# Kernel tuning notes

Hardware: AMD Instinct MI355X
Metric: run time of the kernel (lower is better)

## Reference

```python
import jax, jax.numpy as jnp
from jax import lax
import numpy as np

NUM_CLASS = 80
N_PROP = 256
C_FEAT, H_FEAT, W_FEAT = 1024, 50, 80
IMG_H, IMG_W = 800, 1280
POOL = 14
SPATIAL_SCALE = 0.0625
SCORE_THR = 0.5
NMS_THR = 0.7
K_PRE = 1000   # pre-NMS candidate cap (jit-static stand-in for boolean filter)
K_OUT = 200    # keep[:200] in source
BW = (10.0, 10.0, 5.0, 5.0)
SCALE_CLAMP = float(np.log(1000.0 / 16.0))


def setup_inputs() -> dict:
    key = jax.random.key(0)
    ks = jax.random.split(key, 9)
    features = jax.random.normal(ks[0], (1, C_FEAT, H_FEAT, W_FEAT), jnp.float32)
    x1 = jax.random.uniform(ks[1], (N_PROP,), minval=0.0, maxval=IMG_W - 64.0)
    y1 = jax.random.uniform(ks[2], (N_PROP,), minval=0.0, maxval=IMG_H - 64.0)
    w = jax.random.uniform(ks[3], (N_PROP,), minval=32.0, maxval=320.0)
    h = jax.random.uniform(ks[4], (N_PROP,), minval=32.0, maxval=320.0)
    proposals = jnp.stack([x1, y1, jnp.minimum(x1 + w, float(IMG_W)),
                           jnp.minimum(y1 + h, float(IMG_H))], axis=1)
    d_in = C_FEAT * POOL * POOL
    w_fc = jax.random.normal(ks[5], (d_in, 1024), jnp.float32) / np.sqrt(d_in)
    b_fc = jnp.zeros((1024,), jnp.float32)
    # scale class head up so softmax produces confident (>0.5) detections
    w_cls = jax.random.normal(ks[6], (1024, NUM_CLASS + 1), jnp.float32) * (8.0 / np.sqrt(1024))
    b_cls = jnp.zeros((NUM_CLASS + 1,), jnp.float32)
    w_box = jax.random.normal(ks[7], (1024, NUM_CLASS * 4), jnp.float32) / np.sqrt(1024)
    b_box = jnp.zeros((NUM_CLASS * 4,), jnp.float32)
    return {"features": features, "proposals": proposals, "w_fc": w_fc, "b_fc": b_fc,
            "w_cls": w_cls, "b_cls": b_cls, "w_box": w_box, "b_box": b_box}


def roi_align(features, rois):
    """torchvision RoIAlign (aligned=False), output 14x14, one sample per bin.
    features: [1,C,H,W], rois: [N,4] xyxy. Returns [N,C,14,14]."""
    f = features[0]                               # [C,H,W]
    H, W = f.shape[1], f.shape[2]
    x1 = rois[:, 0] * SPATIAL_SCALE
    y1 = rois[:, 1] * SPATIAL_SCALE
    x2 = rois[:, 2] * SPATIAL_SCALE
    y2 = rois[:, 3] * SPATIAL_SCALE
    rw = jnp.maximum(x2 - x1, 1.0)
    rh = jnp.maximum(y2 - y1, 1.0)
    bw = rw / POOL
    bh = rh / POOL
    grid = jnp.arange(POOL, dtype=jnp.float32) + 0.5
    xs = x1[:, None] + grid[None, :] * bw[:, None]      # [N,P] bin-center x
    ys = y1[:, None] + grid[None, :] * bh[:, None]      # [N,P] bin-center y
    Y = jnp.broadcast_to(ys[:, :, None], (rois.shape[0], POOL, POOL))
    X = jnp.broadcast_to(xs[:, None, :], (rois.shape[0], POOL, POOL))
    valid = (Y >= -1.0) & (Y <= H) & (X >= -1.0) & (X <= W)
    y = jnp.clip(Y, 0.0, H - 1.0)
    x = jnp.clip(X, 0.0, W - 1.0)
    y0 = jnp.floor(y).astype(jnp.int32)
    x0 = jnp.floor(x).astype(jnp.int32)
    y1i = jnp.minimum(y0 + 1, H - 1)
    x1i = jnp.minimum(x0 + 1, W - 1)
    ly = y - y0; lx = x - x0; hy = 1.0 - ly; hx = 1.0 - lx
    g = lambda yi, xi: f[:, yi, xi]               # -> [C,N,P,P]
    val = ((hy * hx) * g(y0, x0) + (hy * lx) * g(y0, x1i)
           + (ly * hx) * g(y1i, x0) + (ly * lx) * g(y1i, x1i))
    val = val * valid.astype(val.dtype)
    return jnp.transpose(val, (1, 0, 2, 3))       # [N,C,P,P]


def apply_deltas(boxes, deltas):
    """boxes,deltas: [..., 4]; detectron-style delta apply with weights BW."""
    w = boxes[..., 2] - boxes[..., 0]
    h = boxes[..., 3] - boxes[..., 1]
    cx = boxes[..., 0] + 0.5 * w
    cy = boxes[..., 1] + 0.5 * h
    dx = deltas[..., 0] / BW[0]
    dy = deltas[..., 1] / BW[1]
    dw = jnp.minimum(deltas[..., 2] / BW[2], SCALE_CLAMP)
    dh = jnp.minimum(deltas[..., 3] / BW[3], SCALE_CLAMP)
    pcx = dx * w + cx
    pcy = dy * h + cy
    pw = jnp.exp(dw) * w
    ph = jnp.exp(dh) * h
    return jnp.stack([pcx - 0.5 * pw, pcy - 0.5 * ph,
                      pcx + 0.5 * pw, pcy + 0.5 * ph], axis=-1)


def _iou_matrix(b):
    area = jnp.maximum(b[:, 2] - b[:, 0], 0.0) * jnp.maximum(b[:, 3] - b[:, 1], 0.0)
    lt = jnp.maximum(b[:, None, :2], b[None, :, :2])
    rb = jnp.minimum(b[:, None, 2:], b[None, :, 2:])
    wh = jnp.clip(rb - lt, 0.0)
    inter = wh[..., 0] * wh[..., 1]
    return inter / jnp.maximum(area[:, None] + area[None, :] - inter, 1e-9)


def forward(features, proposals, w_fc, b_fc, w_cls, b_cls, w_box, b_box):
    feat = roi_align(features, proposals)                 # [N,1024,14,14]
    x = feat.reshape(feat.shape[0], -1) @ w_fc + b_fc     # [N,1024]
    logits = x @ w_cls + b_cls                            # [N,81]
    deltas = x @ w_box + b_box                            # [N,320]
    scores = jax.nn.softmax(logits, axis=-1)[:, 1:]       # [N,80] drop bg

    # per-class box-delta apply (proposal expanded over classes)
    boxes = apply_deltas(jnp.broadcast_to(proposals[:, None, :], (N_PROP, NUM_CLASS, 4)),
                         deltas.reshape(N_PROP, NUM_CLASS, 4))
    boxes = jnp.stack([jnp.clip(boxes[..., 0], 0.0, float(IMG_W)),
                       jnp.clip(boxes[..., 1], 0.0, float(IMG_H)),
                       jnp.clip(boxes[..., 2], 0.0, float(IMG_W)),
                       jnp.clip(boxes[..., 3], 0.0, float(IMG_H))], axis=-1)

    # flatten (proposal, class) candidates; mask = score > 0.5 (boolean filter in source)
    s_flat = scores.reshape(-1)
    b_flat = boxes.reshape(-1, 4)
    c_flat = jnp.broadcast_to(jnp.arange(NUM_CLASS)[None, :], (N_PROP, NUM_CLASS)).reshape(-1)
    masked = jnp.where(s_flat > SCORE_THR, s_flat, -1.0)
    top_s, top_i = lax.top_k(masked, K_PRE)              # score-sorted candidates
    cand_b = b_flat[top_i]
    cand_c = c_flat[top_i]
    cand_valid = top_s > SCORE_THR

    # batched NMS: offset boxes by class so classes never interact
    off = cand_c.astype(jnp.float32) * float(IMG_W + 1)
    iou = _iou_matrix(cand_b + off[:, None])
    idxs = jnp.arange(K_PRE)

    def body(keep, xs):
        i, row = xs
        kept_i = keep[i]
        suppress = kept_i & (row > NMS_THR) & (idxs > i)
        return keep & ~suppress, kept_i

    _, kept = lax.scan(body, cand_valid, (idxs, iou))

    # compact kept candidates (already score-ordered) into top-200 slots
    rank = jnp.cumsum(kept.astype(jnp.int32)) - 1
    slot = jnp.where(kept, rank, K_OUT)  # out-of-range -> dropped
    out_boxes = jnp.zeros((K_OUT, 4), cand_b.dtype).at[slot].set(cand_b, mode='drop')
    out_scores = jnp.zeros((K_OUT,), top_s.dtype).at[slot].set(top_s, mode='drop')
    out_classes = jnp.full((K_OUT,), -1, jnp.int32).at[slot].set(cand_c.astype(jnp.int32), mode='drop')
    return out_boxes, out_scores, out_classes


def reference(features, proposals, w_fc, b_fc, w_cls, b_cls, w_box, b_box):
    return forward(features, proposals, w_fc, b_fc, w_cls, b_cls, w_box, b_box)
```

## Files before the change

### kernel.cpp

```cpp
#include <hip/hip_runtime.h>
#include <math.h>

#define N_PROP 256
#define NUM_CLASS 80
#define H_FEAT 50
#define W_FEAT 80
#define K_DIM 200704
#define D_HID 1024
#define SPATIAL_SCALE 0.0625f
#define SCALE_CLAMP 4.135166556742356f
#define IMG_W_F 1280.0f
#define IMG_H_F 800.0f

typedef unsigned short ushort_t;
typedef __attribute__((ext_vector_type(8))) short short8v;
typedef __attribute__((ext_vector_type(16))) float f32x16;
typedef __attribute__((ext_vector_type(4))) float f32x4v;
typedef __attribute__((ext_vector_type(4))) unsigned short ushort4v;
typedef __attribute__((ext_vector_type(2))) unsigned short ushort2v;

__device__ __forceinline__ unsigned short f2bf(float f) {
  unsigned int u = __builtin_bit_cast(unsigned int, f);
  u += 0x7FFFu + ((u >> 16) & 1u);
  return (unsigned short)(u >> 16);
}
__device__ __forceinline__ float bf2f(unsigned short h) {
  unsigned int u = ((unsigned int)h) << 16;
  return __builtin_bit_cast(float, u);
}

__global__ void roi_kernel(const float* __restrict__ F, const float* __restrict__ props,
                           ushort_t* __restrict__ Ahi, ushort_t* __restrict__ Alo) {
  const int tid = threadIdx.x;
  const int m = blockIdx.y;
  const int cg = blockIdx.x;
  __shared__ float w00[196], w01[196], w10[196], w11[196];
  __shared__ int o00[196], o01[196], o10[196], o11[196];
  const float x1s = props[m*4+0]*SPATIAL_SCALE;
  const float y1s = props[m*4+1]*SPATIAL_SCALE;
  const float x2s = props[m*4+2]*SPATIAL_SCALE;
  const float y2s = props[m*4+3]*SPATIAL_SCALE;
  const float bwf = fmaxf(x2s-x1s, 1.0f) / 14.0f;
  const float bhf = fmaxf(y2s-y1s, 1.0f) / 14.0f;
  if (tid < 196) {
    int ph = tid / 14, pw = tid - ph*14;
    float X = x1s + (pw + 0.5f)*bwf;
    float Y = y1s + (ph + 0.5f)*bhf;
    bool valid = (Y >= -1.0f) && (Y <= (float)H_FEAT) && (X >= -1.0f) && (X <= (float)W_FEAT);
    float x = fminf(fmaxf(X, 0.0f), (float)(W_FEAT-1));
    float y = fminf(fmaxf(Y, 0.0f), (float)(H_FEAT-1));
    float xf = floorf(x), yf = floorf(y);
    int ix0 = (int)xf, iy0 = (int)yf;
    int ix1 = min(ix0+1, W_FEAT-1), iy1 = min(iy0+1, H_FEAT-1);
    float lx = x-xf, ly = y-yf, hx = 1.0f-lx, hy = 1.0f-ly;
    float v = valid ? 1.0f : 0.0f;
    w00[tid] = hy*hx*v; w01[tid] = hy*lx*v; w10[tid] = ly*hx*v; w11[tid] = ly*lx*v;
    o00[tid] = iy0*W_FEAT+ix0; o01[tid] = iy0*W_FEAT+ix1;
    o10[tid] = iy1*W_FEAT+ix0; o11[tid] = iy1*W_FEAT+ix1;
  }
  __syncthreads();
  const int base_c = cg*128;
  const size_t rowbase = (size_t)m*K_DIM + (size_t)base_c*196;
  for (int it = 0; it < 49; ++it) {
    int i2 = it*512 + tid*2;
    int c = i2 / 196;
    int b = i2 - c*196;
    const float* f = F + (size_t)(base_c + c)*4000;
    float v0 = w00[b]*f[o00[b]] + w01[b]*f[o01[b]] + w10[b]*f[o10[b]] + w11[b]*f[o11[b]];
    float v1 = w00[b+1]*f[o00[b+1]] + w01[b+1]*f[o01[b+1]] + w10[b+1]*f[o10[b+1]] + w11[b+1]*f[o11[b+1]];
    unsigned short h0 = f2bf(v0), h1 = f2bf(v1);
    ushort2v hv; hv[0] = h0; hv[1] = h1;
    ushort2v lv; lv[0] = f2bf(v0 - bf2f(h0)); lv[1] = f2bf(v1 - bf2f(h1));
    *(ushort2v*)&Ahi[rowbase + i2] = hv;
    *(ushort2v*)&Alo[rowbase + i2] = lv;
  }
}

__global__ __launch_bounds__(512, 2) void mfma_gemm(
    const ushort_t* __restrict__ Ahi, const ushort_t* __restrict__ Alo,
    const float* __restrict__ B, float* __restrict__ P, int steps_per, int nwg) {
  __shared__ ushort_t lds[32768];
  const int tid = threadIdx.x;
  const int wv = tid >> 6, lane = tid & 63, l31 = lane & 31, lhi = lane >> 5;
  const int wm = wv >> 2, wn = wv & 3;
  int id = blockIdx.x;
  int nid = ((nwg & 7) == 0) ? ((id & 7) * (nwg >> 3) + (id >> 3)) : id;
  const int bn = (nid & 3) * 256;
  const int z  = nid >> 2;
  const int step0 = z * steps_per;
  int steps = steps_per;
  if (step0 + steps > 6272) steps = 6272 - step0;

  f32x16 acc[4][2];
  #pragma unroll
  for (int a = 0; a < 4; ++a)
    #pragma unroll
    for (int b = 0; b < 2; ++b)
      #pragma unroll
      for (int e = 0; e < 16; ++e) acc[a][b][e] = 0.0f;

  if (steps > 0) {
    const int H = steps * 2;
    const ushort_t* asrc[2];
    #pragma unroll
    for (int i = 0; i < 2; ++i) {
      int s = i*512 + tid;
      int plane = s >> 9, kb = (s >> 8) & 1, row = s & 255;
      const ushort_t* basep = plane ? Alo : Ahi;
      asrc[i] = basep + (size_t)row * K_DIM + step0*32 + kb*8;
    }
    const int p = tid >> 6, c4 = tid & 63;
    const bool bstage = (tid < 256);
    const float* bsrc = B + (size_t)(step0*32 + 4*p) * D_HID + bn + c4*4;
    const unsigned bkbh = (unsigned)(p >> 1) * 2048u, bsub = (unsigned)((p & 1) * 4);

    #define STAGE_A(bufn) do { \
      _Pragma("unroll") \
      for (int i = 0; i < 2; ++i) { \
        __builtin_amdgcn_global_load_lds(asrc[i], &lds[(bufn) + (unsigned)(i*512 + tid)*8u], 16, 0, 0); \
        asrc[i] += 16; } \
    } while (0)

    #define LOAD_B() do { \
      if (bstage) { \
        b0 = __builtin_nontemporal_load((const f32x4v*)(bsrc)); \
        b1 = __builtin_nontemporal_load((const f32x4v*)(bsrc + D_HID)); \
        b2 = __builtin_nontemporal_load((const f32x4v*)(bsrc + 2*D_HID)); \
        b3 = __builtin_nontemporal_load((const f32x4v*)(bsrc + 3*D_HID)); \
      } \
      bsrc += 16 * D_HID; \
    } while (0)

    #define WRITE_B(bufn) do { \
      if (bstage) { \
        _Pragma("unroll") \
        for (int cc = 0; cc < 4; ++cc) { \
          float g0 = b0[cc], g1 = b1[cc], g2 = b2[cc], g3 = b3[cc]; \
          ushort4v hv, lv; \
          hv[0]=f2bf(g0); lv[0]=f2bf(g0-bf2f(hv[0])); \
          hv[1]=f2bf(g1); lv[1]=f2bf(g1-bf2f(hv[1])); \
          hv[2]=f2bf(g2); lv[2]=f2bf(g2-bf2f(hv[2])); \
          hv[3]=f2bf(g3); lv[3]=f2bf(g3-bf2f(hv[3])); \
          int col = c4*4 + cc, scol = col ^ ((col>>3)&7); \
          unsigned idx = (bufn) + 8192u + bkbh + (unsigned)scol*8u + bsub; \
          *(ushort4v*)&lds[idx] = hv; \
          *(ushort4v*)&lds[idx + 4096] = lv; \
        } \
      } \
    } while (0)

    #define COMPUTE(bufn) do { \
      short8v ah[4], al[4], bh[2], bl[2]; \
      _Pragma("unroll") \
      for (int ms = 0; ms < 4; ++ms) { \
        unsigned ai = (bufn) + (unsigned)(lhi*2048 + (wm*128 + ms*32 + l31)*8); \
        ah[ms] = *(const short8v*)&lds[ai]; \
        al[ms] = *(const short8v*)&lds[ai + 4096]; \
      } \
      _Pragma("unroll") \
      for (int ns = 0; ns < 2; ++ns) { \
        int col = wn*64 + ns*32 + l31, scol = col ^ ((col>>3)&7); \
        unsigned bi = (bufn) + 8192u + (unsigned)(lhi*2048 + scol*8); \
        bh[ns] = *(const short8v*)&lds[bi]; \
        bl[ns] = *(const short8v*)&lds[bi + 4096]; \
      } \
      __builtin_amdgcn_s_setprio(1); \
      _Pragma("unroll") \
      for (int ms = 0; ms < 4; ++ms) \
        _Pragma("unroll") \
        for (int ns = 0; ns < 2; ++ns) { \
          acc[ms][ns] = __builtin_amdgcn_mfma_f32_32x32x16_bf16(ah[ms], bh[ns], acc[ms][ns], 0, 0, 0); \
          acc[ms][ns] = __builtin_amdgcn_mfma_f32_32x32x16_bf16(ah[ms], bl[ns], acc[ms][ns], 0, 0, 0); \
          acc[ms][ns] = __builtin_amdgcn_mfma_f32_32x32x16_bf16(al[ms], bh[ns], acc[ms][ns], 0, 0, 0); \
        } \
      __builtin_amdgcn_s_setprio(0); \
    } while (0)

    f32x4v b0, b1, b2, b3;
    STAGE_A(0u);
    LOAD_B();
    WRITE_B(0u);
    __syncthreads();
    unsigned cur = 0;
    for (int h = 0; h < H; ++h) {
      const bool last = (h == H - 1);
      if (!last) {
        STAGE_A(cur ^ 16384u);
        LOAD_B();
      }
      COMPUTE(cur);
      if (!last) WRITE_B(cur ^ 16384u);
      __syncthreads();
      cur ^= 16384u;
    }
    #undef STAGE_A
    #undef LOAD_B
    #undef WRITE_B
    #undef COMPUTE
  }
  float* Pp = P + (size_t)z * (N_PROP * D_HID);
  #pragma unroll
  for (int ms = 0; ms < 4; ++ms)
    #pragma unroll
    for (int ns = 0; ns < 2; ++ns)
      #pragma unroll
      for (int r = 0; r < 16; ++r) {
        int row = wm*128 + ms*32 + (r & 3) + 8*(r >> 2) + 4*lhi;
        int col = bn + wn*64 + ns*32 + l31;
        __builtin_nontemporal_store(acc[ms][ns][r], &Pp[(size_t)row * D_HID + col]);
      }
}

__global__ void reduce_kernel(const float* __restrict__ P, float* __restrict__ X, int ksplit) {
  int i = blockIdx.x*256 + threadIdx.x;
  f32x4v s = {0.0f, 0.0f, 0.0f, 0.0f};
  const f32x4v* P4 = (const f32x4v*)P;
  for (int r = 0; r < ksplit; ++r) s += P4[(size_t)r*65536 + i];
  ((f32x4v*)X)[i] = s;
}

__global__ void heads_kernel(const float* __restrict__ X, const float* __restrict__ bfc,
                             const float* __restrict__ wcls, const float* __restrict__ bcls,
                             const float* __restrict__ wbox, const float* __restrict__ bbox,
                             float* __restrict__ scores, float* __restrict__ deltas,
                             float* __restrict__ keym) {
  const int tid = threadIdx.x, m = blockIdx.x;
  __shared__ float xs[1024];
  __shared__ float lg[81];
  __shared__ float red[2];
  #pragma unroll
  for (int r = 0; r < 4; ++r) {
    int k = r*256 + tid;
    xs[k] = X[m*1024 + k] + bfc[k];
  }
  __syncthreads();
  for (int j = tid; j < 401; j += 256) {
    if (j < 81) {
      const float* w = wcls + j;
      float accv = bcls[j];
      #pragma unroll 8
      for (int k = 0; k < 1024; ++k) accv = fmaf(xs[k], w[(size_t)k*81], accv);
      lg[j] = accv;
    } else {
      int jb = j - 81;
      const float* w = wbox + jb;
      float accv = bbox[jb];
      #pragma unroll 8
      for (int k = 0; k < 1024; ++k) accv = fmaf(xs[k], w[(size_t)k*320], accv);
      deltas[m*320 + jb] = accv;
    }
  }
  __syncthreads();
  if (tid == 0) {
    float mx = lg[0]; int amax = 0;
    for (int j = 1; j < 81; ++j) if (lg[j] > mx) { mx = lg[j]; amax = j; }
    float sm = 0.0f;
    for (int j = 0; j < 81; ++j) sm += expf(lg[j]-mx);
    float m2 = -1e30f;
    for (int j = 0; j < 81; ++j) if (j != amax) m2 = fmaxf(m2, lg[j]);
    float s2 = 0.0f;
    for (int j = 0; j < 81; ++j) if (j != amax) s2 += expf(lg[j]-m2);
    keym[m] = (m2 - mx) + logf(s2);
    red[0] = mx; red[1] = sm;
  }
  __syncthreads();
  if (tid < 80) scores[m*80 + tid] = expf(lg[tid+1]-red[0]) / red[1];
}

__global__ void detect_kernel(const float* __restrict__ scores, const float* __restrict__ deltas,
                              const float* __restrict__ props, const float* __restrict__ keym,
                              float* __restrict__ out) {
  const int tid = threadIdx.x;
  __shared__ int s_cnt;
  __shared__ float g_key[256];
  __shared__ float g_score[256];
  __shared__ int   g_idx[256];
  __shared__ float c_score[256];
  __shared__ int   c_idx[256];
  __shared__ float bxs[256][4];
  __shared__ int   bcls[256];
  __shared__ unsigned long long supp[256][4];
  __shared__ unsigned char keptf[256];
  __shared__ short slotv[256];
  if (tid == 0) s_cnt = 0;
  g_key[tid] = 1e30f; g_score[tid] = -1.0f; g_idx[tid] = 0x7FFFFFFF;
  c_score[tid] = -1.0f; c_idx[tid] = 0x7FFFFFFF;
  bxs[tid][0] = bxs[tid][1] = bxs[tid][2] = bxs[tid][3] = 0.0f;
  bcls[tid] = 0; keptf[tid] = 0; slotv[tid] = 0;
  __syncthreads();
  for (int t = 0; t < 80; ++t) {
    int i = t*256 + tid;
    float s = scores[i];
    if (s > 0.5f) {
      int p = atomicAdd(&s_cnt, 1);
      if (p < 256) { g_score[p] = s; g_idx[p] = i; g_key[p] = keym[i/80]; }
    }
  }
  __syncthreads();
  const int C = min(s_cnt, 256);
  if (tid < C) {
    float kt = g_key[tid]; int si = g_idx[tid]; float st = g_score[tid];
    int rank = 0;
    for (int u = 0; u < C; ++u) {
      float ku = g_key[u]; int iu = g_idx[u];
      if ((ku < kt) || (ku == kt && iu < si)) ++rank;
    }
    c_score[rank] = st; c_idx[rank] = si;
  }
  __syncthreads();
  if (tid < C) {
    int fi = c_idx[tid];
    int m = fi / 80, j = fi - m*80;
    float px1 = props[m*4+0], py1 = props[m*4+1], px2 = props[m*4+2], py2 = props[m*4+3];
    float w = px2-px1, h = py2-py1;
    float cx = px1 + 0.5f*w, cy = py1 + 0.5f*h;
    const float* d = deltas + m*320 + j*4;
    float dx = d[0]/10.0f, dy = d[1]/10.0f;
    float dw = fminf(d[2]/5.0f, SCALE_CLAMP), dh = fminf(d[3]/5.0f, SCALE_CLAMP);
    float pcx = dx*w + cx, pcy = dy*h + cy;
    float pw = expf(dw)*w, ph = expf(dh)*h;
    bxs[tid][0] = fminf(fmaxf(pcx - 0.5f*pw, 0.0f), IMG_W_F);
    bxs[tid][1] = fminf(fmaxf(pcy - 0.5f*ph, 0.0f), IMG_H_F);
    bxs[tid][2] = fminf(fmaxf(pcx + 0.5f*pw, 0.0f), IMG_W_F);
    bxs[tid][3] = fminf(fmaxf(pcy + 0.5f*ph, 0.0f), IMG_H_F);
    bcls[tid] = j;
  }
  __syncthreads();
  unsigned long long row[4] = {0,0,0,0};
  if (tid < C) {
    float ax1=bxs[tid][0], ay1=bxs[tid][1], ax2=bxs[tid][2], ay2=bxs[tid][3];
    float aarea = fmaxf(ax2-ax1,0.f)*fmaxf(ay2-ay1,0.f);
    int acl = bcls[tid];
    for (int j2 = tid+1; j2 < C; ++j2) {
      if (bcls[j2] != acl) continue;
      float b1=bxs[j2][0], b2=bxs[j2][1], b3=bxs[j2][2], b4=bxs[j2][3];
      float barea = fmaxf(b3-b1,0.f)*fmaxf(b4-b2,0.f);
      float iw = fmaxf(fminf(ax2,b3) - fmaxf(ax1,b1), 0.f);
      float ih = fmaxf(fminf(ay2,b4) - fmaxf(ay1,b2), 0.f);
      float inter = iw*ih;
      float iou = inter / fmaxf(aarea + barea - inter, 1e-9f);
      if (iou > 0.7f) row[j2>>6] |= (1ull << (j2 & 63));
    }
  }
  supp[tid][0]=row[0]; supp[tid][1]=row[1]; supp[tid][2]=row[2]; supp[tid][3]=row[3];
  __syncthreads();
  if (tid == 0) {
    unsigned long long rem[4] = {0,0,0,0};
    int oc = 0;
    for (int i = 0; i < C; ++i) {
      if ((rem[i>>6] >> (i & 63)) & 1ull) continue;
      keptf[i] = 1; slotv[i] = (short)oc;
      ++oc;
      rem[0]|=supp[i][0]; rem[1]|=supp[i][1]; rem[2]|=supp[i][2]; rem[3]|=supp[i][3];
    }
  }
  __syncthreads();
  for (int i = tid; i < 1200; i += 256) out[i] = (i >= 1000) ? -1.0f : 0.0f;
  __syncthreads();
  if (tid < C && keptf[tid] && slotv[tid] < 200) {
    int oc = slotv[tid];
    out[oc*4+0]=bxs[tid][0]; out[oc*4+1]=bxs[tid][1];
    out[oc*4+2]=bxs[tid][2]; out[oc*4+3]=bxs[tid][3];
    out[800+oc]  = c_score[tid];
    out[1000+oc] = (float)bcls[tid];
  }
}

extern "C" void kernel_launch(void* const* d_in, const int* in_sizes, int n_in,
                              void* d_out, int out_size, void* d_ws, size_t ws_size,
                              hipStream_t stream) {
  const float* F     = (const float*)d_in[0];
  const float* props = (const float*)d_in[1];
  const float* wfc   = (const float*)d_in[2];
  const float* bfc   = (const float*)d_in[3];
  const float* wcls  = (const float*)d_in[4];
  const float* bcls  = (const float*)d_in[5];
  const float* wbox  = (const float*)d_in[6];
  const float* bbox  = (const float*)d_in[7];
  float* out = (float*)d_out;
  char* wsb  = (char*)d_ws;

  const size_t abytes = (size_t)N_PROP * K_DIM * 2;
  ushort_t* Ahi = (ushort_t*)wsb;
  ushort_t* Alo = (ushort_t*)(wsb + abytes);
  float* X  = (float*)(wsb + 2*abytes);
  float* SC = X + 262144;
  float* DL = SC + 20480;
  float* KM = DL + 81920;
  float* P  = KM + 256;
  const size_t fixed = 2*abytes + (size_t)(262144 + 20480 + 81920 + 256) * 4;
  if (ws_size < fixed + 2u*1048576u) {
    (void)hipMemsetAsync(d_out, 0x7F, (size_t)out_size*sizeof(float), stream);
    return;
  }
  int ksplit = (int)((ws_size - fixed) / ((size_t)N_PROP * D_HID * 4));
  if (ksplit > 128) ksplit = 128;
  if (ksplit >= 8) ksplit &= ~7;
  const int steps_per = (6272 + ksplit - 1) / ksplit;
  const int nwg = 4 * ksplit;

  roi_kernel   <<<dim3(8, N_PROP),    256, 0, stream>>>(F, props, Ahi, Alo);
  mfma_gemm    <<<nwg,                512, 0, stream>>>(Ahi, Alo, wfc, P, steps_per, nwg);
  reduce_kernel<<<256,                256, 0, stream>>>(P, X, ksplit);
  heads_kernel <<<N_PROP,             256, 0, stream>>>(X, bfc, wcls, bcls, wbox, bbox, SC, DL, KM);
  detect_kernel<<<1,                  256, 0, stream>>>(SC, DL, props, KM, out);
}
```

Before: 851.6 us.

## Fuse split-K reduction into heads kernel, widen RoI stores, cap ksplit at 64

Drops the separate reduce kernel. The heads kernel now sums the split-K partials straight from P, which removes one launch and the X buffer round trip. The RoI kernel now covers 256 channels per block and writes 4-element bf16 vectors in place of pairs, halving the grid. The split-K cap falls from 128 to 64, which gives fewer partials to reduce but less GEMM parallelism.

```diff
diff --git a/kernel.cpp b/kernel.cpp
--- a/kernel.cpp
+++ b/kernel.cpp
@@ -17,7 +17,6 @@
 typedef __attribute__((ext_vector_type(16))) float f32x16;
 typedef __attribute__((ext_vector_type(4))) float f32x4v;
 typedef __attribute__((ext_vector_type(4))) unsigned short ushort4v;
-typedef __attribute__((ext_vector_type(2))) unsigned short ushort2v;
 
 __device__ __forceinline__ unsigned short f2bf(float f) {
   unsigned int u = __builtin_bit_cast(unsigned int, f);
@@ -59,20 +58,23 @@
     o10[tid] = iy1*W_FEAT+ix0; o11[tid] = iy1*W_FEAT+ix1;
   }
   __syncthreads();
-  const int base_c = cg*128;
+  const int base_c = cg*256;
   const size_t rowbase = (size_t)m*K_DIM + (size_t)base_c*196;
   for (int it = 0; it < 49; ++it) {
-    int i2 = it*512 + tid*2;
-    int c = i2 / 196;
-    int b = i2 - c*196;
+    int i4 = it*1024 + tid*4;
+    int c = i4 / 196;
+    int b = i4 - c*196;
     const float* f = F + (size_t)(base_c + c)*4000;
-    float v0 = w00[b]*f[o00[b]] + w01[b]*f[o01[b]] + w10[b]*f[o10[b]] + w11[b]*f[o11[b]];
-    float v1 = w00[b+1]*f[o00[b+1]] + w01[b+1]*f[o01[b+1]] + w10[b+1]*f[o10[b+1]] + w11[b+1]*f[o11[b+1]];
-    unsigned short h0 = f2bf(v0), h1 = f2bf(v1);
-    ushort2v hv; hv[0] = h0; hv[1] = h1;
-    ushort2v lv; lv[0] = f2bf(v0 - bf2f(h0)); lv[1] = f2bf(v1 - bf2f(h1));
-    *(ushort2v*)&Ahi[rowbase + i2] = hv;
-    *(ushort2v*)&Alo[rowbase + i2] = lv;
+    ushort4v hv, lv;
+    #pragma unroll
+    for (int e = 0; e < 4; ++e) {
+      int be = b + e;
+      float v = w00[be]*f[o00[be]] + w01[be]*f[o01[be]] + w10[be]*f[o10[be]] + w11[be]*f[o11[be]];
+      unsigned short h = f2bf(v);
+      hv[e] = h; lv[e] = f2bf(v - bf2f(h));
+    }
+    *(ushort4v*)&Ahi[rowbase + i4] = hv;
+    *(ushort4v*)&Alo[rowbase + i4] = lv;
   }
 }
 
@@ -211,15 +213,8 @@
       }
 }
 
-__global__ void reduce_kernel(const float* __restrict__ P, float* __restrict__ X, int ksplit) {
-  int i = blockIdx.x*256 + threadIdx.x;
-  f32x4v s = {0.0f, 0.0f, 0.0f, 0.0f};
-  const f32x4v* P4 = (const f32x4v*)P;
-  for (int r = 0; r < ksplit; ++r) s += P4[(size_t)r*65536 + i];
-  ((f32x4v*)X)[i] = s;
-}
-
-__global__ void heads_kernel(const float* __restrict__ X, const float* __restrict__ bfc,
+__global__ void heads_kernel(const float* __restrict__ P, int ksplit,
+                             const float* __restrict__ bfc,
                              const float* __restrict__ wcls, const float* __restrict__ bcls,
                              const float* __restrict__ wbox, const float* __restrict__ bbox,
                              float* __restrict__ scores, float* __restrict__ deltas,
@@ -229,9 +224,13 @@
   __shared__ float lg[81];
   __shared__ float red[2];
   #pragma unroll
-  for (int r = 0; r < 4; ++r) {
-    int k = r*256 + tid;
-    xs[k] = X[m*1024 + k] + bfc[k];
+  for (int r4 = 0; r4 < 4; ++r4) {
+    int k = r4*256 + tid;
+    float s = bfc[k];
+    const float* Pk = P + (size_t)m*1024 + k;
+    #pragma unroll 4
+    for (int r = 0; r < ksplit; ++r) s += Pk[(size_t)r*(N_PROP*D_HID)];
+    xs[k] = s;
   }
   __syncthreads();
   for (int j = tid; j < 401; j += 256) {
@@ -383,25 +382,23 @@
   const size_t abytes = (size_t)N_PROP * K_DIM * 2;
   ushort_t* Ahi = (ushort_t*)wsb;
   ushort_t* Alo = (ushort_t*)(wsb + abytes);
-  float* X  = (float*)(wsb + 2*abytes);
-  float* SC = X + 262144;
+  float* SC = (float*)(wsb + 2*abytes);
   float* DL = SC + 20480;
   float* KM = DL + 81920;
   float* P  = KM + 256;
-  const size_t fixed = 2*abytes + (size_t)(262144 + 20480 + 81920 + 256) * 4;
+  const size_t fixed = 2*abytes + (size_t)(20480 + 81920 + 256) * 4;
   if (ws_size < fixed + 2u*1048576u) {
     (void)hipMemsetAsync(d_out, 0x7F, (size_t)out_size*sizeof(float), stream);
     return;
   }
   int ksplit = (int)((ws_size - fixed) / ((size_t)N_PROP * D_HID * 4));
-  if (ksplit > 128) ksplit = 128;
+  if (ksplit > 64) ksplit = 64;
   if (ksplit >= 8) ksplit &= ~7;
   const int steps_per = (6272 + ksplit - 1) / ksplit;
   const int nwg = 4 * ksplit;
 
-  roi_kernel   <<<dim3(8, N_PROP),    256, 0, stream>>>(F, props, Ahi, Alo);
+  roi_kernel   <<<dim3(4, N_PROP),    256, 0, stream>>>(F, props, Ahi, Alo);
   mfma_gemm    <<<nwg,                512, 0, stream>>>(Ahi, Alo, wfc, P, steps_per, nwg);
-  reduce_kernel<<<256,                256, 0, stream>>>(P, X, ksplit);
-  heads_kernel <<<N_PROP,             256, 0, stream>>>(X, bfc, wcls, bcls, wbox, bbox, SC, DL, KM);
+  heads_kernel <<<N_PROP,             256, 0, stream>>>(P, ksplit, bfc, wcls, bcls, wbox, bbox, SC, DL, KM);
   detect_kernel<<<1,                  256, 0, stream>>>(SC, DL, props, KM, out);
 }
```

Measured after the change: 852.5 us. About the same (+0.1%).
